# Kernel optimization log

Hardware: AMD Instinct MI355X
Metric: run time of the kernel (lower is better)

The kernel has to match this reference:

```python
import jax, jax.numpy as jnp
import numpy as np

H = 768
R = 24


def setup_inputs() -> dict:
    key = jax.random.key(0)
    ks = jax.random.split(key, 9)
    B, S = 4, 256
    hidden = jax.random.normal(ks[0], (B, S, H), dtype=jnp.float32)
    # ConcatHandshaking fc: Linear(2H -> H); torch weight shape (out,in)=(H,2H)
    fc_w = jax.random.normal(ks[1], (H, 2 * H), dtype=jnp.float32) * (1.0 / np.sqrt(2 * H))
    fc_b = jnp.zeros((H,), dtype=jnp.float32)
    # h2t: Linear(H -> 2)
    h2t_w = jax.random.normal(ks[2], (2, H), dtype=jnp.float32) * (1.0 / np.sqrt(H))
    h2t_b = jnp.zeros((2,), dtype=jnp.float32)
    # h2h / t2t TaggingProjector: R independent Linear(H -> 3), batched as (R,3,H)
    h2h_w = jax.random.normal(ks[3], (R, 3, H), dtype=jnp.float32) * (1.0 / np.sqrt(H))
    h2h_b = jnp.zeros((R, 3), dtype=jnp.float32)
    t2t_w = jax.random.normal(ks[4], (R, 3, H), dtype=jnp.float32) * (1.0 / np.sqrt(H))
    t2t_b = jnp.zeros((R, 3), dtype=jnp.float32)
    return {
        "hidden": hidden,
        "fc_w": fc_w, "fc_b": fc_b,
        "h2t_w": h2t_w, "h2t_b": h2t_b,
        "h2h_w": h2h_w, "h2h_b": h2h_b,
        "t2t_w": t2t_w, "t2t_b": t2t_b,
    }


def _handshaking(hidden, fc_w, fc_b):
    # hidden: (B, S, H). Pairs (i, j) with i <= j in row-major (torch loop) order.
    S = hidden.shape[1]
    idx_i, idx_j = jnp.triu_indices(S)  # each (P,), P = S(S+1)/2
    # concat([h_i, h_j]) @ W^T == h_i @ Wl^T + h_j @ Wr^T  (avoids (B,P,2H) buffer)
    Wl = fc_w[:, :H]  # (H, H)
    Wr = fc_w[:, H:]  # (H, H)
    left = jnp.einsum('bsh,oh->bso', hidden, Wl)   # (B, S, H)
    right = jnp.einsum('bsh,oh->bso', hidden, Wr)  # (B, S, H)
    hs = jnp.tanh(left[:, idx_i, :] + right[:, idx_j, :] + fc_b)  # (B, P, H)
    return hs


def reference(hidden, fc_w, fc_b, h2t_w, h2t_b, h2h_w, h2h_b, t2t_w, t2t_b):
    hs = _handshaking(hidden, fc_w, fc_b)  # (B, P, H)
    # h2t: plain Linear(H->2), logits (no softmax in original)
    h2t = jnp.einsum('bph,oh->bpo', hs, h2t_w) + h2t_b  # (B, P, 2)
    # TaggingProjector: batched per-relation Linear(H->3), then softmax over tags
    h2h = jax.nn.softmax(jnp.einsum('bph,rth->brpt', hs, h2h_w) + h2h_b[None, :, None, :], axis=-1)
    t2t = jax.nn.softmax(jnp.einsum('bph,rth->brpt', hs, t2t_w) + t2t_b[None, :, None, :], axis=-1)
    return (h2t, h2h, t2t)
```

## Files before the change

kernel.cpp:

```cpp
#include <hip/hip_runtime.h>
#include <hip/hip_bf16.h>

#define H 768
#define SEQ 256
#define NPAIR 32896
#define NTOT 131584
#define NOUTP 160
#define OFF_H2H 263168u
#define OFF_T2T 9737216u

#define N_BPK 122880
#define SCL 2.8853900817779268f

#define CH 64
#define NCH 12
#define BSLOT 24576
#define SLAB_STR 166

typedef short bf16x8 __attribute__((ext_vector_type(8)));
typedef float f32x4 __attribute__((ext_vector_type(4)));
typedef float f32x16 __attribute__((ext_vector_type(16)));

__device__ __forceinline__ float tanh_s(float xs) {
    float e = __builtin_amdgcn_exp2f(xs);
    return fmaf(-2.0f, __builtin_amdgcn_rcpf(e + 1.0f), 1.0f);
}
__device__ __forceinline__ float bf_lo(int w){ return __uint_as_float(((unsigned)w) << 16); }
__device__ __forceinline__ float bf_hi(int w){ return __uint_as_float(((unsigned)w) & 0xffff0000u); }
__device__ __forceinline__ float bfu(unsigned short u){ return __uint_as_float(((unsigned)u) << 16); }
__device__ __forceinline__ int cvtpk(float lo, float hi) {
    int r;
    asm("v_cvt_pk_bf16_f32 %0, %1, %2" : "=v"(r) : "v"(lo), "v"(hi));
    return r;
}
__device__ __forceinline__ unsigned short bf16r(float x){
    unsigned int u = __float_as_uint(x);
    u += 0x7fffu + ((u >> 16) & 1u);
    return (unsigned short)(u >> 16);
}
__device__ __forceinline__ bf16x8 tanh_frag(int4 lv, int4 rv) {
    int4 st;
    st.x = cvtpk(tanh_s(bf_lo(lv.x) + bf_lo(rv.x)), tanh_s(bf_hi(lv.x) + bf_hi(rv.x)));
    st.y = cvtpk(tanh_s(bf_lo(lv.y) + bf_lo(rv.y)), tanh_s(bf_hi(lv.y) + bf_hi(rv.y)));
    st.z = cvtpk(tanh_s(bf_lo(lv.z) + bf_lo(rv.z)), tanh_s(bf_hi(lv.z) + bf_hi(rv.z)));
    st.w = cvtpk(tanh_s(bf_lo(lv.w) + bf_lo(rv.w)), tanh_s(bf_hi(lv.w) + bf_hi(rv.w)));
    return __builtin_bit_cast(bf16x8, st);
}

typedef const __attribute__((address_space(1))) unsigned int* as1_u32p;
typedef __attribute__((address_space(3))) unsigned int* as3_u32p;
__device__ __forceinline__ void gload_lds16(const void* g, void* l) {
    __builtin_amdgcn_global_load_lds((as1_u32p)g, (as3_u32p)l, 16, 0, 0);
}

__device__ __forceinline__ int row_start(int i) { return i * SEQ - (i * (i - 1)) / 2; }
__device__ __forceinline__ void pair_ij(int p, int& oi, int& oj) {
    double disc = 263169.0 - 8.0 * (double)p;
    int i = (int)((513.0 - sqrt(disc)) * 0.5);
    if (i > 0 && row_start(i) > p) --i;
    while (row_start(i + 1) <= p) ++i;
    oi = i;
    oj = i + (p - row_start(i));
}
__device__ __forceinline__ int batch_of(int g) {
    return (g >= 3 * NPAIR) ? 3 : (g >= 2 * NPAIR) ? 2 : (g >= NPAIR) ? 1 : 0;
}

__global__ __launch_bounds__(256) void pack_kernel(
    const float* __restrict__ h2t_w, const float* __restrict__ h2h_w,
    const float* __restrict__ t2t_w, const float* __restrict__ h2t_b,
    const float* __restrict__ h2h_b, const float* __restrict__ t2t_b,
    unsigned short* __restrict__ Bpk, float* __restrict__ bc)
{
    int idx = blockIdx.x * 256 + threadIdx.x;
    if (idx < N_BPK) {
        int j = idx & 7, lane = (idx >> 3) & 63, rest = idx >> 9;
        int fr = rest % 20, c = rest / 20;
        int s = fr / 5, f = fr % 5;
        int n = f * 32 + (lane & 31);
        int k = c * CH + s * 16 + ((lane >> 5) << 3) + j;
        float v = 0.f;
        if (n < 2)        v = h2t_w[n * H + k];
        else if (n < 74)  v = h2h_w[(n - 2) * H + k];
        else if (n < 146) v = t2t_w[(n - 74) * H + k];
        Bpk[c * 12288 + (idx - c * 10240)] = bf16r(v);
    } else if (idx < N_BPK + NOUTP) {
        int q = idx - N_BPK;
        float v = 0.f;
        if (q < 2)        v = h2t_b[q];
        else if (q < 74)  v = h2h_b[q - 2];
        else if (q < 146) v = t2t_b[q - 74];
        bc[q] = v;
    }
}

__global__ __launch_bounds__(256, 2) void lr_mfma(
    const float* __restrict__ hidden, const float* __restrict__ fc_w,
    const float* __restrict__ fc_b,
    unsigned short* __restrict__ LB, unsigned short* __restrict__ RB)
{
    __shared__ __align__(16) char sm[16384];
    const int tid = threadIdx.x, l = tid & 63, w = tid >> 6;
    const int wm = w >> 1, wn = w & 1;
    const int m0 = blockIdx.x * 64, n0 = blockIdx.y * 64;
    f32x4 acc[2][2] = {};
    for (int c = 0; c < 12; ++c) {
        const int k0 = c * 64;
        #pragma unroll
        for (int it = 0; it < 2; ++it) {
            int idx = tid + it * 256;
            int row = idx >> 3, k8 = idx & 7;
            const float4* src = reinterpret_cast<const float4*>(hidden + (size_t)(m0 + row) * H + k0 + k8 * 8);
            float4 a = src[0], bq = src[1];
            int4 st;
            st.x = cvtpk(a.x, a.y);  st.y = cvtpk(a.z, a.w);
            st.z = cvtpk(bq.x, bq.y); st.w = cvtpk(bq.z, bq.w);
            *reinterpret_cast<int4*>(sm + row * 128 + ((k8 * 16) ^ ((row & 7) << 4))) = st;
        }
        #pragma unroll
        for (int it = 0; it < 2; ++it) {
            int idx = tid + it * 256;
            int row = idx >> 3, k8 = idx & 7;
            const float* fsrc = (n0 < H)
                ? fc_w + (size_t)(n0 + row) * (2 * H) + k0 + k8 * 8
                : fc_w + (size_t)(n0 - H + row) * (2 * H) + H + k0 + k8 * 8;
            const float4* src = reinterpret_cast<const float4*>(fsrc);
            float4 a = src[0], bq = src[1];
            int4 st;
            st.x = cvtpk(a.x, a.y);  st.y = cvtpk(a.z, a.w);
            st.z = cvtpk(bq.x, bq.y); st.w = cvtpk(bq.z, bq.w);
            *reinterpret_cast<int4*>(sm + 8192 + row * 128 + ((k8 * 16) ^ ((row & 7) << 4))) = st;
        }
        __syncthreads();
        #pragma unroll
        for (int kk = 0; kk < 2; ++kk) {
            const int sl = kk * 4 + (l >> 4);
            const int swz = (l & 7) << 4;
            bf16x8 af[2], bfr[2];
            #pragma unroll
            for (int a = 0; a < 2; ++a) {
                int row = 32 * wm + 16 * a + (l & 15);
                af[a] = *reinterpret_cast<const bf16x8*>(sm + row * 128 + ((sl * 16) ^ swz));
            }
            #pragma unroll
            for (int f = 0; f < 2; ++f) {
                int row = 32 * wn + 16 * f + (l & 15);
                bfr[f] = *reinterpret_cast<const bf16x8*>(sm + 8192 + row * 128 + ((sl * 16) ^ swz));
            }
            #pragma unroll
            for (int a = 0; a < 2; ++a)
                #pragma unroll
                for (int f = 0; f < 2; ++f)
                    acc[a][f] = __builtin_amdgcn_mfma_f32_16x16x32_bf16(af[a], bfr[f], acc[a][f], 0, 0, 0);
        }
        __syncthreads();
    }
    #pragma unroll
    for (int a = 0; a < 2; ++a)
        #pragma unroll
        for (int f = 0; f < 2; ++f)
            #pragma unroll
            for (int r = 0; r < 4; ++r) {
                int row = m0 + 32 * wm + 16 * a + 4 * (l >> 4) + r;
                int col = n0 + 32 * wn + 16 * f + (l & 15);
                float v = acc[a][f][r];
                if (n0 < H) LB[(size_t)row * H + col] = bf16r((v + fc_b[col]) * SCL);
                else        RB[(size_t)row * H + (col - H)] = bf16r(v * SCL);
            }
}

__global__ __launch_bounds__(256) void pair_mfma(
    const unsigned short* __restrict__ LB, const unsigned short* __restrict__ RB,
    const unsigned short* __restrict__ Bpk, const float* __restrict__ bc,
    float* __restrict__ out)
{
    __shared__ __align__(16) char sm[49792];
    float* bc_s = reinterpret_cast<float*>(sm + 49152);

    const int tid = threadIdx.x, l = tid & 63, w = tid >> 6;
    const int g0 = blockIdx.x * 128;
    const int b = batch_of(g0);
    const int p0 = g0 - b * NPAIR;

    if (tid < NOUTP) bc_s[tid] = bc[tid];

    const int row = 32 * w + (l & 31);
    int pi, pj;
    pair_ij(p0 + row, pi, pj);
    const int kb = (l >> 5) << 3;
    const unsigned short* lp = LB + (size_t)(b * SEQ + pi) * H + kb;
    const unsigned short* rp = RB + (size_t)(b * SEQ + pj) * H + kb;

    const char* bpk = reinterpret_cast<const char*>(Bpk);
    const int soff = w * 1024 + l * 16;
    const int doff = w * 1024;

    f32x16 acc[5] = {};

    {
        #pragma unroll
        for (int r = 0; r < 5; ++r)
            gload_lds16(bpk + r * 4096 + soff, sm + r * 4096 + doff);
        __builtin_amdgcn_sched_barrier(0);
    }
    int4 lv0 = *reinterpret_cast<const int4*>(lp);
    int4 lv1 = *reinterpret_cast<const int4*>(lp + 16);
    int4 lv2 = *reinterpret_cast<const int4*>(lp + 32);
    int4 lv3 = *reinterpret_cast<const int4*>(lp + 48);
    int4 rv0 = *reinterpret_cast<const int4*>(rp);
    int4 rv1 = *reinterpret_cast<const int4*>(rp + 16);
    int4 rv2 = *reinterpret_cast<const int4*>(rp + 32);
    int4 rv3 = *reinterpret_cast<const int4*>(rp + 48);
    asm volatile("s_waitcnt vmcnt(8) lgkmcnt(0)" ::: "memory");
    __builtin_amdgcn_s_barrier();
    __builtin_amdgcn_sched_barrier(0);

    #pragma unroll 2
    for (int c = 0; c < NCH - 1; ++c) {
        char* bufn = sm + (((c + 1) & 1) ? BSLOT : 0);
        const char* bn = bpk + (c + 1) * BSLOT;
        #pragma unroll
        for (int r = 0; r < 5; ++r)
            gload_lds16(bn + r * 4096 + soff, bufn + r * 4096 + doff);
        __builtin_amdgcn_sched_barrier(0);
        bf16x8 a0 = tanh_frag(lv0, rv0);
        bf16x8 a1 = tanh_frag(lv1, rv1);
        bf16x8 a2 = tanh_frag(lv2, rv2);
        bf16x8 a3 = tanh_frag(lv3, rv3);
        const int co = (c + 1) * CH;
        lv0 = *reinterpret_cast<const int4*>(lp + co);
        lv1 = *reinterpret_cast<const int4*>(lp + co + 16);
        lv2 = *reinterpret_cast<const int4*>(lp + co + 32);
        lv3 = *reinterpret_cast<const int4*>(lp + co + 48);
        rv0 = *reinterpret_cast<const int4*>(rp + co);
        rv1 = *reinterpret_cast<const int4*>(rp + co + 16);
        rv2 = *reinterpret_cast<const int4*>(rp + co + 32);
        rv3 = *reinterpret_cast<const int4*>(rp + co + 48);
        const char* bufc = sm + ((c & 1) ? BSLOT : 0);
        #pragma unroll
        for (int f = 0; f < 5; ++f) {
            bf16x8 bfr = *reinterpret_cast<const bf16x8*>(bufc + ((0 * 5 + f) * 64 + l) * 16);
            acc[f] = __builtin_amdgcn_mfma_f32_32x32x16_bf16(a0, bfr, acc[f], 0, 0, 0);
        }
        #pragma unroll
        for (int f = 0; f < 5; ++f) {
            bf16x8 bfr = *reinterpret_cast<const bf16x8*>(bufc + ((1 * 5 + f) * 64 + l) * 16);
            acc[f] = __builtin_amdgcn_mfma_f32_32x32x16_bf16(a1, bfr, acc[f], 0, 0, 0);
        }
        #pragma unroll
        for (int f = 0; f < 5; ++f) {
            bf16x8 bfr = *reinterpret_cast<const bf16x8*>(bufc + ((2 * 5 + f) * 64 + l) * 16);
            acc[f] = __builtin_amdgcn_mfma_f32_32x32x16_bf16(a2, bfr, acc[f], 0, 0, 0);
        }
        #pragma unroll
        for (int f = 0; f < 5; ++f) {
            bf16x8 bfr = *reinterpret_cast<const bf16x8*>(bufc + ((3 * 5 + f) * 64 + l) * 16);
            acc[f] = __builtin_amdgcn_mfma_f32_32x32x16_bf16(a3, bfr, acc[f], 0, 0, 0);
        }
        asm volatile("s_waitcnt vmcnt(8) lgkmcnt(0)" ::: "memory");
        __builtin_amdgcn_s_barrier();
        __builtin_amdgcn_sched_barrier(0);
    }
    {
        bf16x8 a0 = tanh_frag(lv0, rv0);
        bf16x8 a1 = tanh_frag(lv1, rv1);
        bf16x8 a2 = tanh_frag(lv2, rv2);
        bf16x8 a3 = tanh_frag(lv3, rv3);
        const char* bufc = sm + BSLOT;
        #pragma unroll
        for (int f = 0; f < 5; ++f) {
            bf16x8 bfr = *reinterpret_cast<const bf16x8*>(bufc + ((0 * 5 + f) * 64 + l) * 16);
            acc[f] = __builtin_amdgcn_mfma_f32_32x32x16_bf16(a0, bfr, acc[f], 0, 0, 0);
        }
        #pragma unroll
        for (int f = 0; f < 5; ++f) {
            bf16x8 bfr = *reinterpret_cast<const bf16x8*>(bufc + ((1 * 5 + f) * 64 + l) * 16);
            acc[f] = __builtin_amdgcn_mfma_f32_32x32x16_bf16(a1, bfr, acc[f], 0, 0, 0);
        }
        #pragma unroll
        for (int f = 0; f < 5; ++f) {
            bf16x8 bfr = *reinterpret_cast<const bf16x8*>(bufc + ((2 * 5 + f) * 64 + l) * 16);
            acc[f] = __builtin_amdgcn_mfma_f32_32x32x16_bf16(a2, bfr, acc[f], 0, 0, 0);
        }
        #pragma unroll
        for (int f = 0; f < 5; ++f) {
            bf16x8 bfr = *reinterpret_cast<const bf16x8*>(bufc + ((3 * 5 + f) * 64 + l) * 16);
            acc[f] = __builtin_amdgcn_mfma_f32_32x32x16_bf16(a3, bfr, acc[f], 0, 0, 0);
        }
    }
    asm volatile("s_waitcnt lgkmcnt(0)" ::: "memory");
    __builtin_amdgcn_s_barrier();

    unsigned short* slab = reinterpret_cast<unsigned short*>(sm);
    #pragma unroll
    for (int f = 0; f < 5; ++f)
        #pragma unroll
        for (int g = 0; g < 16; ++g) {
            int rw = 32 * w + (g & 3) + 8 * (g >> 2) + 4 * (l >> 5);
            slab[rw * SLAB_STR + f * 32 + (l & 31)] = bf16r(acc[f][g]);
        }
    __syncthreads();

    {
        int pr = tid >> 1, tt = tid & 1;
        float val = bfu(slab[pr * SLAB_STR + tt]) + bc_s[tt];
        __builtin_nontemporal_store(val, &out[(size_t)(g0 + pr) * 2 + tt]);
    }
    #pragma unroll
    for (int it = 0; it < 24; ++it) {
        int item = it * 256 + tid;
        int pr = item & 127, rr = item >> 7;
        int p = p0 + pr;
        int ob = 2 + rr * 3;
        const unsigned short* sp = slab + pr * SLAB_STR + ob;
        float l0 = bfu(sp[0]) + bc_s[ob + 0];
        float l1 = bfu(sp[1]) + bc_s[ob + 1];
        float l2 = bfu(sp[2]) + bc_s[ob + 2];
        float mx = fmaxf(l0, fmaxf(l1, l2));
        float e0 = __expf(l0 - mx), e1 = __expf(l1 - mx), e2 = __expf(l2 - mx);
        float inv = __fdividef(1.0f, e0 + e1 + e2);
        size_t base = (rr < 24)
            ? (size_t)OFF_H2H + ((size_t)(b * 24 + rr) * NPAIR + p) * 3
            : (size_t)OFF_T2T + ((size_t)(b * 24 + rr - 24) * NPAIR + p) * 3;
        __builtin_nontemporal_store(e0 * inv, &out[base + 0]);
        __builtin_nontemporal_store(e1 * inv, &out[base + 1]);
        __builtin_nontemporal_store(e2 * inv, &out[base + 2]);
    }
}

extern "C" void kernel_launch(void* const* d_in, const int* in_sizes, int n_in,
                              void* d_out, int out_size, void* d_ws, size_t ws_size,
                              hipStream_t stream) {
    const float* hidden = (const float*)d_in[0];
    const float* fc_w   = (const float*)d_in[1];
    const float* fc_b   = (const float*)d_in[2];
    const float* h2t_w  = (const float*)d_in[3];
    const float* h2t_b  = (const float*)d_in[4];
    const float* h2h_w  = (const float*)d_in[5];
    const float* h2h_b  = (const float*)d_in[6];
    const float* t2t_w  = (const float*)d_in[7];
    const float* t2t_b  = (const float*)d_in[8];

    char* wsb = (char*)d_ws;
    unsigned short* LBw  = (unsigned short*)(wsb);
    unsigned short* RBw  = (unsigned short*)(wsb + 1572864);
    unsigned short* Bpk  = (unsigned short*)(wsb + 3145728);
    float*          bc   = (float*)        (wsb + 3440640);

    float* out = (float*)d_out;

    pack_kernel<<<(N_BPK + NOUTP + 255) / 256, 256, 0, stream>>>(
        h2t_w, h2h_w, t2t_w, h2t_b, h2h_b, t2t_b, Bpk, bc);
    lr_mfma<<<dim3(16, 24), 256, 0, stream>>>(hidden, fc_w, fc_b, LBw, RBw);
    pair_mfma<<<NTOT / 128, 256, 0, stream>>>(LBw, RBw, Bpk, bc, out);
}
```

Before: 95.75 us.

## Split pair kernel into producer and consumer warps for tanh and MFMA

The pair kernel goes from 256 to 512 threads. Four producer waves gather the L/R rows, compute tanh into double-buffered LDS A tiles and stream B weight chunks into LDS. Four consumer waves run only the MFMA loop, with both sides synchronised by s_barrier each chunk. The aim is to overlap the transcendental and gather work with matrix math, at the cost of more LDS, a larger block that may lower occupancy, and an extra LDS round trip for A.

```diff
diff --git a/kernel.cpp b/kernel.cpp
--- a/kernel.cpp
+++ b/kernel.cpp
@@ -14,8 +14,11 @@
 
 #define CH 64
 #define NCH 12
-#define BSLOT 24576
+#define BCH 20480
 #define SLAB_STR 166
+
+#define LDS_B0 32768
+#define LDS_BC 73728
 
 typedef short bf16x8 __attribute__((ext_vector_type(8)));
 typedef float f32x4 __attribute__((ext_vector_type(4)));
@@ -38,13 +41,13 @@
     u += 0x7fffu + ((u >> 16) & 1u);
     return (unsigned short)(u >> 16);
 }
-__device__ __forceinline__ bf16x8 tanh_frag(int4 lv, int4 rv) {
+__device__ __forceinline__ int4 tanh_pack(int4 lv, int4 rv) {
     int4 st;
     st.x = cvtpk(tanh_s(bf_lo(lv.x) + bf_lo(rv.x)), tanh_s(bf_hi(lv.x) + bf_hi(rv.x)));
     st.y = cvtpk(tanh_s(bf_lo(lv.y) + bf_lo(rv.y)), tanh_s(bf_hi(lv.y) + bf_hi(rv.y)));
     st.z = cvtpk(tanh_s(bf_lo(lv.z) + bf_lo(rv.z)), tanh_s(bf_hi(lv.z) + bf_hi(rv.z)));
     st.w = cvtpk(tanh_s(bf_lo(lv.w) + bf_lo(rv.w)), tanh_s(bf_hi(lv.w) + bf_hi(rv.w)));
-    return __builtin_bit_cast(bf16x8, st);
+    return st;
 }
 
 typedef const __attribute__((address_space(1))) unsigned int* as1_u32p;
@@ -83,7 +86,7 @@
         if (n < 2)        v = h2t_w[n * H + k];
         else if (n < 74)  v = h2h_w[(n - 2) * H + k];
         else if (n < 146) v = t2t_w[(n - 74) * H + k];
-        Bpk[c * 12288 + (idx - c * 10240)] = bf16r(v);
+        Bpk[idx] = bf16r(v);
     } else if (idx < N_BPK + NOUTP) {
         int q = idx - N_BPK;
         float v = 0.f;
@@ -169,13 +172,13 @@
             }
 }
 
-__global__ __launch_bounds__(256) void pair_mfma(
+__global__ __launch_bounds__(512, 4) void pair_mfma(
     const unsigned short* __restrict__ LB, const unsigned short* __restrict__ RB,
     const unsigned short* __restrict__ Bpk, const float* __restrict__ bc,
     float* __restrict__ out)
 {
-    __shared__ __align__(16) char sm[49792];
-    float* bc_s = reinterpret_cast<float*>(sm + 49152);
+    __shared__ __align__(16) char sm[74368];
+    float* bc_s = reinterpret_cast<float*>(sm + LDS_BC);
 
     const int tid = threadIdx.x, l = tid & 63, w = tid >> 6;
     const int g0 = blockIdx.x * 128;
@@ -184,131 +187,120 @@
 
     if (tid < NOUTP) bc_s[tid] = bc[tid];
 
-    const int row = 32 * w + (l & 31);
-    int pi, pj;
-    pair_ij(p0 + row, pi, pj);
-    const int kb = (l >> 5) << 3;
-    const unsigned short* lp = LB + (size_t)(b * SEQ + pi) * H + kb;
-    const unsigned short* rp = RB + (size_t)(b * SEQ + pj) * H + kb;
-
-    const char* bpk = reinterpret_cast<const char*>(Bpk);
-    const int soff = w * 1024 + l * 16;
-    const int doff = w * 1024;
-
-    f32x16 acc[5] = {};
-
-    {
+    const bool producer = (w >= 4);
+    const int half = l >> 5;
+
+    if (producer) {
+        const int pw = w - 4;
+        const int row = 32 * pw + (l & 31);
+        int pi, pj;
+        pair_ij(p0 + row, pi, pj);
+        const int kb = half << 3;
+        const unsigned short* lp = LB + (size_t)(b * SEQ + pi) * H + kb;
+        const unsigned short* rp = RB + (size_t)(b * SEQ + pj) * H + kb;
+        const char* bsrc = reinterpret_cast<const char*>(Bpk) + pw * 1024 + l * 16;
+        const int bdoff = pw * 1024;
+        const int abase = half * 2048 + row * 16;
+
+        int4 lv0, lv1, lv2, lv3, rv0, rv1, rv2, rv3;
+
         #pragma unroll
         for (int r = 0; r < 5; ++r)
-            gload_lds16(bpk + r * 4096 + soff, sm + r * 4096 + doff);
+            gload_lds16(bsrc + r * 4096, sm + LDS_B0 + bdoff + r * 4096);
         __builtin_amdgcn_sched_barrier(0);
-    }
-    int4 lv0 = *reinterpret_cast<const int4*>(lp);
-    int4 lv1 = *reinterpret_cast<const int4*>(lp + 16);
-    int4 lv2 = *reinterpret_cast<const int4*>(lp + 32);
-    int4 lv3 = *reinterpret_cast<const int4*>(lp + 48);
-    int4 rv0 = *reinterpret_cast<const int4*>(rp);
-    int4 rv1 = *reinterpret_cast<const int4*>(rp + 16);
-    int4 rv2 = *reinterpret_cast<const int4*>(rp + 32);
-    int4 rv3 = *reinterpret_cast<const int4*>(rp + 48);
-    asm volatile("s_waitcnt vmcnt(8) lgkmcnt(0)" ::: "memory");
-    __builtin_amdgcn_s_barrier();
-    __builtin_amdgcn_sched_barrier(0);
-
-    #pragma unroll 2
-    for (int c = 0; c < NCH - 1; ++c) {
-        char* bufn = sm + (((c + 1) & 1) ? BSLOT : 0);
-        const char* bn = bpk + (c + 1) * BSLOT;
-        #pragma unroll
-        for (int r = 0; r < 5; ++r)
-            gload_lds16(bn + r * 4096 + soff, bufn + r * 4096 + doff);
-        __builtin_amdgcn_sched_barrier(0);
-        bf16x8 a0 = tanh_frag(lv0, rv0);
-        bf16x8 a1 = tanh_frag(lv1, rv1);
-        bf16x8 a2 = tanh_frag(lv2, rv2);
-        bf16x8 a3 = tanh_frag(lv3, rv3);
-        const int co = (c + 1) * CH;
-        lv0 = *reinterpret_cast<const int4*>(lp + co);
-        lv1 = *reinterpret_cast<const int4*>(lp + co + 16);
-        lv2 = *reinterpret_cast<const int4*>(lp + co + 32);
-        lv3 = *reinterpret_cast<const int4*>(lp + co + 48);
-        rv0 = *reinterpret_cast<const int4*>(rp + co);
-        rv1 = *reinterpret_cast<const int4*>(rp + co + 16);
-        rv2 = *reinterpret_cast<const int4*>(rp + co + 32);
-        rv3 = *reinterpret_cast<const int4*>(rp + co + 48);
-        const char* bufc = sm + ((c & 1) ? BSLOT : 0);
-        #pragma unroll
-        for (int f = 0; f < 5; ++f) {
-            bf16x8 bfr = *reinterpret_cast<const bf16x8*>(bufc + ((0 * 5 + f) * 64 + l) * 16);
-            acc[f] = __builtin_amdgcn_mfma_f32_32x32x16_bf16(a0, bfr, acc[f], 0, 0, 0);
-        }
-        #pragma unroll
-        for (int f = 0; f < 5; ++f) {
-            bf16x8 bfr = *reinterpret_cast<const bf16x8*>(bufc + ((1 * 5 + f) * 64 + l) * 16);
-            acc[f] = __builtin_amdgcn_mfma_f32_32x32x16_bf16(a1, bfr, acc[f], 0, 0, 0);
-        }
-        #pragma unroll
-        for (int f = 0; f < 5; ++f) {
-            bf16x8 bfr = *reinterpret_cast<const bf16x8*>(bufc + ((2 * 5 + f) * 64 + l) * 16);
-            acc[f] = __builtin_amdgcn_mfma_f32_32x32x16_bf16(a2, bfr, acc[f], 0, 0, 0);
-        }
-        #pragma unroll
-        for (int f = 0; f < 5; ++f) {
-            bf16x8 bfr = *reinterpret_cast<const bf16x8*>(bufc + ((3 * 5 + f) * 64 + l) * 16);
-            acc[f] = __builtin_amdgcn_mfma_f32_32x32x16_bf16(a3, bfr, acc[f], 0, 0, 0);
-        }
+        lv0 = *reinterpret_cast<const int4*>(lp);
+        lv1 = *reinterpret_cast<const int4*>(lp + 16);
+        lv2 = *reinterpret_cast<const int4*>(lp + 32);
+        lv3 = *reinterpret_cast<const int4*>(lp + 48);
+        rv0 = *reinterpret_cast<const int4*>(rp);
+        rv1 = *reinterpret_cast<const int4*>(rp + 16);
+        rv2 = *reinterpret_cast<const int4*>(rp + 32);
+        rv3 = *reinterpret_cast<const int4*>(rp + 48);
+        {
+            char* adst = sm + abase;
+            *reinterpret_cast<int4*>(adst)         = tanh_pack(lv0, rv0);
+            *reinterpret_cast<int4*>(adst + 4096)  = tanh_pack(lv1, rv1);
+            *reinterpret_cast<int4*>(adst + 8192)  = tanh_pack(lv2, rv2);
+            *reinterpret_cast<int4*>(adst + 12288) = tanh_pack(lv3, rv3);
+        }
+        lv0 = *reinterpret_cast<const int4*>(lp + CH);
+        lv1 = *reinterpret_cast<const int4*>(lp + CH + 16);
+        lv2 = *reinterpret_cast<const int4*>(lp + CH + 32);
+        lv3 = *reinterpret_cast<const int4*>(lp + CH + 48);
+        rv0 = *reinterpret_cast<const int4*>(rp + CH);
+        rv1 = *reinterpret_cast<const int4*>(rp + CH + 16);
+        rv2 = *reinterpret_cast<const int4*>(rp + CH + 32);
+        rv3 = *reinterpret_cast<const int4*>(rp + CH + 48);
         asm volatile("s_waitcnt vmcnt(8) lgkmcnt(0)" ::: "memory");
         __builtin_amdgcn_s_barrier();
         __builtin_amdgcn_sched_barrier(0);
-    }
-    {
-        bf16x8 a0 = tanh_frag(lv0, rv0);
-        bf16x8 a1 = tanh_frag(lv1, rv1);
-        bf16x8 a2 = tanh_frag(lv2, rv2);
-        bf16x8 a3 = tanh_frag(lv3, rv3);
-        const char* bufc = sm + BSLOT;
-        #pragma unroll
-        for (int f = 0; f < 5; ++f) {
-            bf16x8 bfr = *reinterpret_cast<const bf16x8*>(bufc + ((0 * 5 + f) * 64 + l) * 16);
-            acc[f] = __builtin_amdgcn_mfma_f32_32x32x16_bf16(a0, bfr, acc[f], 0, 0, 0);
-        }
-        #pragma unroll
-        for (int f = 0; f < 5; ++f) {
-            bf16x8 bfr = *reinterpret_cast<const bf16x8*>(bufc + ((1 * 5 + f) * 64 + l) * 16);
-            acc[f] = __builtin_amdgcn_mfma_f32_32x32x16_bf16(a1, bfr, acc[f], 0, 0, 0);
-        }
-        #pragma unroll
-        for (int f = 0; f < 5; ++f) {
-            bf16x8 bfr = *reinterpret_cast<const bf16x8*>(bufc + ((2 * 5 + f) * 64 + l) * 16);
-            acc[f] = __builtin_amdgcn_mfma_f32_32x32x16_bf16(a2, bfr, acc[f], 0, 0, 0);
-        }
-        #pragma unroll
-        for (int f = 0; f < 5; ++f) {
-            bf16x8 bfr = *reinterpret_cast<const bf16x8*>(bufc + ((3 * 5 + f) * 64 + l) * 16);
-            acc[f] = __builtin_amdgcn_mfma_f32_32x32x16_bf16(a3, bfr, acc[f], 0, 0, 0);
-        }
-    }
-    asm volatile("s_waitcnt lgkmcnt(0)" ::: "memory");
-    __builtin_amdgcn_s_barrier();
+
+        for (int c = 0; c < NCH - 1; ++c) {
+            const char* bn = bsrc + (size_t)(c + 1) * BCH;
+            char* bbufn = sm + LDS_B0 + (((c + 1) & 1) ? BCH : 0) + bdoff;
+            #pragma unroll
+            for (int r = 0; r < 5; ++r)
+                gload_lds16(bn + r * 4096, bbufn + r * 4096);
+            __builtin_amdgcn_sched_barrier(0);
+            char* adst = sm + (((c + 1) & 1) ? 16384 : 0) + abase;
+            *reinterpret_cast<int4*>(adst)         = tanh_pack(lv0, rv0);
+            *reinterpret_cast<int4*>(adst + 4096)  = tanh_pack(lv1, rv1);
+            *reinterpret_cast<int4*>(adst + 8192)  = tanh_pack(lv2, rv2);
+            *reinterpret_cast<int4*>(adst + 12288) = tanh_pack(lv3, rv3);
+            const int co = ((c + 2 < NCH) ? (c + 2) : (NCH - 1)) * CH;
+            lv0 = *reinterpret_cast<const int4*>(lp + co);
+            lv1 = *reinterpret_cast<const int4*>(lp + co + 16);
+            lv2 = *reinterpret_cast<const int4*>(lp + co + 32);
+            lv3 = *reinterpret_cast<const int4*>(lp + co + 48);
+            rv0 = *reinterpret_cast<const int4*>(rp + co);
+            rv1 = *reinterpret_cast<const int4*>(rp + co + 16);
+            rv2 = *reinterpret_cast<const int4*>(rp + co + 32);
+            rv3 = *reinterpret_cast<const int4*>(rp + co + 48);
+            asm volatile("s_waitcnt vmcnt(8) lgkmcnt(0)" ::: "memory");
+            __builtin_amdgcn_s_barrier();
+            __builtin_amdgcn_sched_barrier(0);
+        }
+        __builtin_amdgcn_s_barrier();
+    } else {
+        const int arow16 = (32 * w + (l & 31)) * 16;
+        f32x16 acc[5] = {};
+        __builtin_amdgcn_s_barrier();
+        for (int c = 0; c < NCH; ++c) {
+            const char* abuf = sm + ((c & 1) ? 16384 : 0);
+            const char* bbuf = sm + LDS_B0 + ((c & 1) ? BCH : 0);
+            #pragma unroll
+            for (int s = 0; s < 4; ++s) {
+                bf16x8 af = *reinterpret_cast<const bf16x8*>(abuf + s * 4096 + half * 2048 + arow16);
+                #pragma unroll
+                for (int f = 0; f < 5; ++f) {
+                    bf16x8 bfr = *reinterpret_cast<const bf16x8*>(bbuf + ((s * 5 + f) * 64 + l) * 16);
+                    acc[f] = __builtin_amdgcn_mfma_f32_32x32x16_bf16(af, bfr, acc[f], 0, 0, 0);
+                }
+            }
+            asm volatile("s_waitcnt lgkmcnt(0)" ::: "memory");
+            __builtin_amdgcn_sched_barrier(0);
+            __builtin_amdgcn_s_barrier();
+        }
+        unsigned short* slab = reinterpret_cast<unsigned short*>(sm);
+        #pragma unroll
+        for (int f = 0; f < 5; ++f)
+            #pragma unroll
+            for (int g = 0; g < 16; ++g) {
+                int rw = 32 * w + (g & 3) + 8 * (g >> 2) + 4 * half;
+                slab[rw * SLAB_STR + f * 32 + (l & 31)] = bf16r(acc[f][g]);
+            }
+    }
+    __syncthreads();
 
     unsigned short* slab = reinterpret_cast<unsigned short*>(sm);
-    #pragma unroll
-    for (int f = 0; f < 5; ++f)
-        #pragma unroll
-        for (int g = 0; g < 16; ++g) {
-            int rw = 32 * w + (g & 3) + 8 * (g >> 2) + 4 * (l >> 5);
-            slab[rw * SLAB_STR + f * 32 + (l & 31)] = bf16r(acc[f][g]);
-        }
-    __syncthreads();
-
-    {
+    if (tid < 256) {
         int pr = tid >> 1, tt = tid & 1;
         float val = bfu(slab[pr * SLAB_STR + tt]) + bc_s[tt];
         __builtin_nontemporal_store(val, &out[(size_t)(g0 + pr) * 2 + tt]);
     }
     #pragma unroll
-    for (int it = 0; it < 24; ++it) {
-        int item = it * 256 + tid;
+    for (int it = 0; it < 12; ++it) {
+        int item = it * 512 + tid;
         int pr = item & 127, rr = item >> 7;
         int p = p0 + pr;
         int ob = 2 + rr * 3;
@@ -345,12 +337,12 @@
     unsigned short* LBw  = (unsigned short*)(wsb);
     unsigned short* RBw  = (unsigned short*)(wsb + 1572864);
     unsigned short* Bpk  = (unsigned short*)(wsb + 3145728);
-    float*          bc   = (float*)        (wsb + 3440640);
+    float*          bc   = (float*)        (wsb + 3391488);
 
     float* out = (float*)d_out;
 
     pack_kernel<<<(N_BPK + NOUTP + 255) / 256, 256, 0, stream>>>(
         h2t_w, h2h_w, t2t_w, h2t_b, h2h_b, t2t_b, Bpk, bc);
     lr_mfma<<<dim3(16, 24), 256, 0, stream>>>(hidden, fc_w, fc_b, LBw, RBw);
-    pair_mfma<<<NTOT / 128, 256, 0, stream>>>(LBw, RBw, Bpk, bc, out);
-}
+    pair_mfma<<<NTOT / 128, 512, 0, stream>>>(LBw, RBw, Bpk, bc, out);
+}
```

Result: slower. 99.65 us (+4.1%).
